# Kernel optimization log

Measured on AMD Instinct MI355X. Metric: run time of the kernel, lower is better.

## Reference

```python
import jax, jax.numpy as jnp
import numpy as np

D_IN = 2048
D_SAE = 16384
BATCH = 4096


def setup_inputs() -> dict:
    key = jax.random.key(0)
    kx, kw, kb, kt, kd = jax.random.split(key, 5)
    x = jax.random.normal(kx, (BATCH, D_IN), dtype=jnp.float32)
    # kaiming-uniform-like init for encoder weight [d_sae, d_in]
    bound = float(np.sqrt(6.0 / D_IN))
    W_enc = jax.random.uniform(kw, (D_SAE, D_IN), minval=-bound, maxval=bound, dtype=jnp.float32)
    b_enc = jnp.zeros((D_SAE,), dtype=jnp.float32)
    # decoder weight [d_in, d_sae]; use small random values instead of the
    # zeros init so the reference output is non-degenerate
    W_dec = jax.random.normal(kd, (D_IN, D_SAE), dtype=jnp.float32) * 0.02
    # learnable per-feature thresholds tau (tau_init=0.0 plus jitter)
    tau = jax.random.normal(kt, (D_SAE,), dtype=jnp.float32) * 0.01
    return {"x": x, "W_enc": W_enc, "b_enc": b_enc, "tau": tau, "W_dec": W_dec, "k_cap": 64}


def reference(x, W_enc, b_enc, tau, W_dec, k_cap):
    # encode: pre = x @ W_enc.T + b_enc  -> [B, d_sae]
    pre = jnp.einsum('bi,si->bs', x, W_enc) + b_enc
    # JumpReLU gate: y = relu(pre - tau), mask = (pre > tau)
    codes = jax.nn.relu(pre - tau)
    mask = (pre > tau).astype(pre.dtype)
    # top-k cap (gate_mode='jumprelu_cap'): keep codes >= k-th largest per row
    k = min(k_cap, codes.shape[1])
    vals = jax.lax.top_k(codes, k)[0]          # [B, k], sorted desc
    kth = vals[:, -1:]                          # [B, 1]
    mask_k = (codes >= kth).astype(codes.dtype)
    codes = codes * mask_k
    mask = mask * mask_k
    # decode: recon = codes @ W_dec.T  -> [B, d_in]
    recon = jnp.einsum('bs,is->bi', codes, W_dec)
    return recon, codes, mask
```

## Files before the change

### kernel.cpp

```cpp
#include <hip/hip_runtime.h>

#define D_IN   2048
#define D_SAE  16384
#define BATCH  4096
#define CAP    256
#define MAXB   64
#define DELTA  1e-2f

typedef __attribute__((ext_vector_type(8))) _Float16 f16x8;
typedef __attribute__((ext_vector_type(4))) _Float16 f16x4;
typedef __attribute__((ext_vector_type(4))) float f32x4;

__global__ __launch_bounds__(256) void to_f16_2(const float* __restrict__ in1,
                                                ushort* __restrict__ out1, int n14,
                                                const float* __restrict__ in2,
                                                ushort* __restrict__ out2, int n24) {
    int i = blockIdx.x * blockDim.x + threadIdx.x;
    int stride = gridDim.x * blockDim.x;
    int total = n14 + n24;
    for (; i < total; i += stride) {
        const float4* src = (i < n14) ? ((const float4*)in1 + i)
                                      : ((const float4*)in2 + (i - n14));
        ushort4* dst = (i < n14) ? ((ushort4*)out1 + i)
                                 : ((ushort4*)out2 + (i - n14));
        float4 v = *src;
        ushort4 h;
        float*  vp = (float*)&v;
        ushort* hp = (ushort*)&h;
        #pragma unroll
        for (int j = 0; j < 4; ++j) {
            _Float16 f = (_Float16)vp[j];
            hp[j] = *(ushort*)&f;
        }
        *dst = h;
    }
}

__device__ __forceinline__ void async_copy16(const void* g, void* l) {
    __builtin_amdgcn_global_load_lds(
        (const __attribute__((address_space(1))) unsigned int*)g,
        (__attribute__((address_space(3))) unsigned int*)l, 16, 0, 0);
}

template<int F16OUT>
__global__ __launch_bounds__(512) void gemm_enc_mfma(
        const ushort* __restrict__ xh,
        const ushort* __restrict__ wh,
        const float* __restrict__ b_enc,
        const float* __restrict__ tau,
        void* __restrict__ rawout) {
    __shared__ ushort lds9[9][8192];

    const int tid  = threadIdx.x;
    const int w    = tid >> 6;
    const int lane = tid & 63;
    const int wm   = w >> 2;
    const int wn   = w & 3;
    const int m0 = blockIdx.x * 256;
    const int s0 = blockIdx.y * 256;

    const int fr = lane & 15;
    const int fq = lane >> 4;

    const int srow0 = w * 8 + (lane >> 3);
    const int srow1 = 64 + srow0;
    const int sc0i  = (((lane & 7) - srow0) & 7) * 8;

    const ushort* panelA = xh + (size_t)m0 * 2048;
    const ushort* panelB = wh + (size_t)s0 * 2048;

    auto stage_unit = [&](int slot, int ab, int h, int koff) {
        const ushort* gp = (ab == 0) ? panelA : panelB;
        const ushort* g0 = gp + (size_t)(h * 128 + srow0) * 2048 + koff + sc0i;
        const ushort* g1 = gp + (size_t)(h * 128 + srow1) * 2048 + koff + sc0i;
        async_copy16(g0, &lds9[slot][w * 512]);
        async_copy16(g1, &lds9[slot][4096 + w * 512]);
    };

    int a_off[8][2], b_off[4][2];
    #pragma unroll
    for (int m = 0; m < 8; ++m) {
        int r = m * 16 + fr;
        #pragma unroll
        for (int kk = 0; kk < 2; ++kk)
            a_off[m][kk] = r * 64 + (((kk * 4 + fq) + r) & 7) * 8;
    }
    #pragma unroll
    for (int g = 0; g < 4; ++g) {
        int r = (wn & 1) * 64 + g * 16 + fr;
        #pragma unroll
        for (int kk = 0; kk < 2; ++kk)
            b_off[g][kk] = r * 64 + (((kk * 4 + fq) + r) & 7) * 8;
    }

    f32x4 acc[8][4] = {};

    stage_unit(0, 0, 0, 0);
    stage_unit(1, 1, 0, 0);
    stage_unit(2, 1, 1, 0);
    stage_unit(3, 0, 1, 0);
    stage_unit(4, 0, 0, 64);

    const int wmu = wm ? 3 : 0;
    const int wbu = 1 + (wn >> 1);

#define STG(P)                                                                 \
    do {                                                                       \
        int u_ = 4 * t + (P) + 5;                                              \
        if (u_ < 128) {                                                        \
            int ui_ = u_ & 3;                                                  \
            stage_unit(u_ % 9, (ui_ == 0 || ui_ == 3) ? 0 : 1,                 \
                       (ui_ >= 2) ? 1 : 0, (u_ >> 2) * 64);                    \
        }                                                                      \
    } while (0)

#define PHASE(QM, QN, P)                                                       \
    do {                                                                       \
        STG(P);                                                                \
        if ((P) == 0) {                                                        \
            if (t != 31) asm volatile("s_waitcnt vmcnt(4)" ::: "memory");      \
            else         asm volatile("s_waitcnt vmcnt(0)" ::: "memory");      \
        }                                                                      \
        asm volatile("s_barrier" ::: "memory");                                \
        f16x8 af[4][2], bf[2][2];                                              \
        _Pragma("unroll") for (int mm = 0; mm < 4; ++mm)                       \
            _Pragma("unroll") for (int kk = 0; kk < 2; ++kk)                   \
                af[mm][kk] = *(const f16x8*)&ldsA[a_off[(QM) * 4 + mm][kk]];   \
        _Pragma("unroll") for (int nn = 0; nn < 2; ++nn)                       \
            _Pragma("unroll") for (int kk = 0; kk < 2; ++kk)                   \
                bf[nn][kk] = *(const f16x8*)&ldsB[b_off[(QN) * 2 + nn][kk]];   \
        __builtin_amdgcn_s_setprio(1);                                         \
        _Pragma("unroll") for (int kk = 0; kk < 2; ++kk)                       \
            _Pragma("unroll") for (int mm = 0; mm < 4; ++mm)                   \
                _Pragma("unroll") for (int nn = 0; nn < 2; ++nn)               \
                    acc[(QM) * 4 + mm][(QN) * 2 + nn] =                        \
                        __builtin_amdgcn_mfma_f32_16x16x32_f16(                \
                            af[mm][kk], bf[nn][kk],                            \
                            acc[(QM) * 4 + mm][(QN) * 2 + nn], 0, 0, 0);       \
        __builtin_amdgcn_s_setprio(0);                                         \
        asm volatile("s_barrier" ::: "memory");                                \
    } while (0)

    for (int t = 0; t < 32; ++t) {
        const ushort* ldsA = &lds9[(4 * t + wmu) % 9][0];
        const ushort* ldsB = &lds9[(4 * t + wbu) % 9][0];
        PHASE(0, 0, 0);
        PHASE(0, 1, 1);
        PHASE(1, 0, 2);
        PHASE(1, 1, 3);
    }
#undef PHASE
#undef STG

    float bias[4];
    int col[4];
    #pragma unroll
    for (int n = 0; n < 4; ++n) {
        col[n] = s0 + wn * 64 + n * 16 + fr;
        bias[n] = b_enc[col[n]] - tau[col[n]];
    }
    #pragma unroll
    for (int m = 0; m < 8; ++m) {
        int rbase = m0 + wm * 128 + m * 16 + fq * 4;
        #pragma unroll
        for (int n = 0; n < 4; ++n) {
            #pragma unroll
            for (int r = 0; r < 4; ++r) {
                float v = fmaxf(acc[m][n][r] + bias[n], 0.f);
                size_t ofs = (size_t)(rbase + r) * D_SAE + col[n];
                if (F16OUT) {
                    _Float16 hv = (_Float16)v;
                    ((ushort*)rawout)[ofs] = *(ushort*)&hv;
                } else {
                    ((float*)rawout)[ofs] = v;
                }
            }
        }
    }
}

__global__ __launch_bounds__(256) void transpose_wdec_f16(const float* __restrict__ W_dec,
                                                          _Float16* __restrict__ W_decT) {
    __shared__ float t[64][65];
    const int tid = threadIdx.x;
    const int x0 = blockIdx.x * 64;
    const int y0 = blockIdx.y * 64;
    const int tx = tid & 15;
    const int ty = tid >> 4;
    #pragma unroll
    for (int p = 0; p < 4; ++p) {
        float4 v = *(const float4*)&W_dec[(size_t)(y0 + p * 16 + ty) * D_SAE + x0 + tx * 4];
        t[p * 16 + ty][tx * 4 + 0] = v.x;
        t[p * 16 + ty][tx * 4 + 1] = v.y;
        t[p * 16 + ty][tx * 4 + 2] = v.z;
        t[p * 16 + ty][tx * 4 + 3] = v.w;
    }
    __syncthreads();
    #pragma unroll
    for (int p = 0; p < 4; ++p) {
        int s = p * 16 + ty;
        f16x4 o;
        #pragma unroll
        for (int q = 0; q < 4; ++q)
            o[q] = (_Float16)t[tx * 4 + q][s];
        *(f16x4*)&W_decT[(size_t)(x0 + s) * D_IN + y0 + tx * 4] = o;
    }
}

__device__ __forceinline__ int block_incl_scan(int v, int tid, int* wtot, int* pT) {
    const int lane = tid & 63, wid = tid >> 6;
    int s = v;
    #pragma unroll
    for (int off = 1; off < 64; off <<= 1) {
        int n = __shfl_up(s, off, 64);
        if (lane >= off) s += n;
    }
    if (lane == 63) wtot[wid] = s;
    __syncthreads();
    int pre = 0, T = 0;
    #pragma unroll
    for (int w2 = 0; w2 < 4; ++w2) {
        int t = wtot[w2];
        T += t;
        if (w2 < wid) pre += t;
    }
    __syncthreads();
    *pT = T;
    return s + pre;
}

template<int SRC16>
__global__ __launch_bounds__(256) void select_apply(
        const void* __restrict__ rawsrc,
        float* __restrict__ codes, float* __restrict__ mask,
        const int* __restrict__ kptr,
        const float* __restrict__ x, const float* __restrict__ W_enc,
        const float* __restrict__ b_enc, const float* __restrict__ tau,
        int* __restrict__ cnt_out, int* __restrict__ idx_out,
        float* __restrict__ val_out) {
    const int row = blockIdx.x;
    const int tid = threadIdx.x;
    const int wid = tid >> 6;
    const long base = (long)row * D_SAE;

    float c[8][8];
    if (SRC16) {
        const ushort* rh = (const ushort*)rawsrc;
        #pragma unroll
        for (int i = 0; i < 8; ++i) {
            uint4 u = *(const uint4*)(rh + base + i * 2048 + tid * 8);
            const unsigned* up = (const unsigned*)&u;
            #pragma unroll
            for (int q = 0; q < 4; ++q) {
                ushort b0 = (ushort)(up[q] & 0xFFFFu), b1 = (ushort)(up[q] >> 16);
                _Float16 h0, h1;
                *(ushort*)&h0 = b0; *(ushort*)&h1 = b1;
                c[i][2 * q]     = (float)h0;
                c[i][2 * q + 1] = (float)h1;
            }
        }
    } else {
        const float* rf = (const float*)rawsrc;
        #pragma unroll
        for (int i = 0; i < 8; ++i) {
            float4 v0 = *(const float4*)(rf + base + i * 2048 + tid * 8);
            float4 v1 = *(const float4*)(rf + base + i * 2048 + tid * 8 + 4);
            c[i][0] = v0.x; c[i][1] = v0.y; c[i][2] = v0.z; c[i][3] = v0.w;
            c[i][4] = v1.x; c[i][5] = v1.y; c[i][6] = v1.z; c[i][7] = v1.w;
        }
    }

    int K = kptr[0];
    if (K > D_SAE) K = D_SAE;

    __shared__ int    hist4[4][1024];
    __shared__ int    hist1c[64];
    __shared__ int    wtot[4];
    __shared__ int    bidx[MAXB];
    __shared__ double exactv[MAXB];
    __shared__ int    selfl[MAXB];
    __shared__ double dsum[4];
    __shared__ int    sh_B, sh_nAB, sh_kpat;

    #pragma unroll
    for (int q = 0; q < 16; ++q) ((int*)hist4)[tid + q * 256] = 0;
    if (tid < 64) hist1c[tid] = 0;
    if (tid == 0) { sh_B = -1; sh_nAB = 0; }
    __syncthreads();
    #pragma unroll
    for (int i = 0; i < 8; ++i)
        #pragma unroll
        for (int j = 0; j < 8; ++j) {
            _Float16 h = (_Float16)c[i][j];
            ushort pat = *(ushort*)&h;
            if (pat) atomicAdd(&hist4[wid][pat >> 6], 1);
        }
    __syncthreads();

    int mh[4];
    int s_loc = 0;
    #pragma unroll
    for (int q = 0; q < 4; ++q) {
        mh[q] = hist4[0][4 * tid + q] + hist4[1][4 * tid + q]
              + hist4[2][4 * tid + q] + hist4[3][4 * tid + q];
        s_loc += mh[q];
    }
    int T1;
    int incl1 = block_incl_scan(s_loc, tid, wtot, &T1);
    int I = T1 - (incl1 - s_loc);
    int E = I - s_loc;
    if (I >= K && E < K) {
        int cnt = E, b;
        for (b = 3; b > 0; --b) {
            cnt += mh[b];
            if (cnt >= K) break;
        }
        if (cnt < K) { cnt += mh[0]; b = 0; }
        sh_B = 4 * tid + b;
        sh_nAB = cnt - mh[b];
    }
    __syncthreads();
    const int B = sh_B, nAB = sh_nAB;

    if (B >= 0) {
        #pragma unroll
        for (int i = 0; i < 8; ++i)
            #pragma unroll
            for (int j = 0; j < 8; ++j) {
                _Float16 h = (_Float16)c[i][j];
                ushort pat = *(ushort*)&h;
                if (pat && (int)(pat >> 6) == B) atomicAdd(&hist1c[pat & 63], 1);
            }
    }
    __syncthreads();
    if (tid == 0) {
        int kpat = 0;
        if (B >= 0) {
            int cnt = nAB, l;
            for (l = 63; l >= 0; --l) {
                cnt += hist1c[l];
                if (cnt >= K) break;
            }
            if (l < 0) l = 0;
            kpat = (B << 6) | l;
        }
        sh_kpat = kpat;
    }
    __syncthreads();
    _Float16 kh; *(ushort*)&kh = (ushort)sh_kpat;
    const float kf = (float)kh;
    const float thr_hi = kf + DELTA;
    const float thr_lo = kf - DELTA;

    int cA = 0, cB2 = 0;
    #pragma unroll
    for (int i = 0; i < 8; ++i)
        #pragma unroll
        for (int j = 0; j < 8; ++j) {
            float cc = c[i][j];
            cA  += (cc > thr_hi);
            cB2 += (cc >= thr_lo) && (cc <= thr_hi);
        }
    int pv = (cB2 << 16) | cA;
    int T2;
    int incl2 = block_incl_scan(pv, tid, wtot, &T2);
    int excl2 = incl2 - pv;
    const int nA = T2 & 0xFFFF;
    int posB = excl2 >> 16;
    int nb   = T2 >> 16;
    if (nb > MAXB) nb = MAXB;

    {
        int p = posB;
        #pragma unroll
        for (int i = 0; i < 8; ++i)
            #pragma unroll
            for (int j = 0; j < 8; ++j) {
                float cc = c[i][j];
                if ((cc >= thr_lo) && (cc <= thr_hi)) {
                    if (p < MAXB) bidx[p] = i * 2048 + tid * 8 + j;
                    ++p;
                }
            }
    }
    __syncthreads();

    const float* xrow = x + (size_t)row * D_IN;
    for (int jj = 0; jj < nb; ++jj) {
        int s = bidx[jj];
        const float* wrow = W_enc + (size_t)s * D_IN;
        double a = 0.0;
        #pragma unroll
        for (int q = 0; q < 8; ++q)
            a += (double)xrow[tid * 8 + q] * (double)wrow[tid * 8 + q];
        #pragma unroll
        for (int off = 32; off; off >>= 1) a += __shfl_xor(a, off, 64);
        if ((tid & 63) == 0) dsum[tid >> 6] = a;
        __syncthreads();
        if (tid == 0)
            exactv[jj] = dsum[0] + dsum[1] + dsum[2] + dsum[3]
                         + (double)b_enc[s] - (double)tau[s];
        __syncthreads();
    }

    int m = K - nA;
    if (m > nb) m = nb;
    if (tid < nb) {
        double e = exactv[tid];
        int rank = 0;
        for (int l = 0; l < nb; ++l) rank += (exactv[l] > e);
        selfl[tid] = (rank < m) ? 1 : 0;
    }
    __syncthreads();

    unsigned long long ov = 0ull;
    for (int jj = 0; jj < nb; ++jj) {
        int s = bidx[jj];
        if (((s >> 3) & 255) == tid && selfl[jj])
            ov |= 1ull << (((s >> 11) << 3) | (s & 7));
    }

    int kc = 0;
    #pragma unroll
    for (int i = 0; i < 8; ++i)
        #pragma unroll
        for (int j = 0; j < 8; ++j) {
            float cc = c[i][j];
            bool sel = (cc > thr_hi) || ((ov >> (i * 8 + j)) & 1ull);
            kc += sel && (cc > 0.f);
        }
    int T3;
    int incl3 = block_incl_scan(kc, tid, wtot, &T3);
    int pos   = incl3 - kc;
    int total = T3;

    #pragma unroll
    for (int i = 0; i < 8; ++i) {
        f32x4 cf0, cf1, mf0, mf1;
        #pragma unroll
        for (int j = 0; j < 8; ++j) {
            float cc = c[i][j];
            bool sel = (cc > thr_hi) || ((ov >> (i * 8 + j)) & 1ull);
            bool m_  = sel && (cc > 0.f);
            float cv = sel ? cc : 0.f;
            float mv = m_ ? 1.f : 0.f;
            if (j < 4) { cf0[j] = cv; mf0[j] = mv; }
            else       { cf1[j - 4] = cv; mf1[j - 4] = mv; }
            if (m_) {
                if (pos < CAP) {
                    idx_out[row * CAP + pos] = i * 2048 + tid * 8 + j;
                    val_out[row * CAP + pos] = cv;
                }
                ++pos;
            }
        }
        long o = base + i * 2048 + tid * 8;
        __builtin_nontemporal_store(cf0, (f32x4*)(codes + o));
        __builtin_nontemporal_store(cf1, (f32x4*)(codes + o + 4));
        __builtin_nontemporal_store(mf0, (f32x4*)(mask + o));
        __builtin_nontemporal_store(mf1, (f32x4*)(mask + o + 4));
    }
    if (tid == 0) cnt_out[row] = total < CAP ? total : CAP;
}

__global__ __launch_bounds__(256) void recon_sparse(const _Float16* __restrict__ Wd16,
                                                    const int* __restrict__ cnt,
                                                    const int* __restrict__ idx,
                                                    const float* __restrict__ val,
                                                    float* __restrict__ recon) {
    const int row  = blockIdx.x >> 1;
    const int half = blockIdx.x & 1;
    const int tid  = threadIdx.x;
    __shared__ int   s_idx[CAP];
    __shared__ float s_val[CAP];
    const int n = cnt[row];
    for (int j = tid; j < n; j += 256) {
        s_idx[j] = idx[row * CAP + j];
        s_val[j] = val[row * CAP + j];
    }
    __syncthreads();

    const int colb = half * 1024 + tid * 4;
    float4 a = {0.f, 0.f, 0.f, 0.f};
    for (int j = 0; j < n; ++j) {
        float c = s_val[j];
        f16x4 w0 = *(const f16x4*)(Wd16 + (size_t)s_idx[j] * D_IN + colb);
        a.x = fmaf(c, (float)w0[0], a.x); a.y = fmaf(c, (float)w0[1], a.y);
        a.z = fmaf(c, (float)w0[2], a.z); a.w = fmaf(c, (float)w0[3], a.w);
    }
    *(float4*)(recon + (size_t)row * D_IN + colb) = a;
}

extern "C" void kernel_launch(void* const* d_in, const int* in_sizes, int n_in,
                              void* d_out, int out_size, void* d_ws, size_t ws_size,
                              hipStream_t stream) {
    const float* x     = (const float*)d_in[0];
    const float* W_enc = (const float*)d_in[1];
    const float* b_enc = (const float*)d_in[2];
    const float* tau   = (const float*)d_in[3];
    const float* W_dec = (const float*)d_in[4];
    const int*   kptr  = (const int*)d_in[5];

    float* recon = (float*)d_out;
    float* codes = recon + (size_t)BATCH * D_IN;
    float* maskp = codes + (size_t)BATCH * D_SAE;

    char* w = (char*)d_ws;
    const size_t OFF_X   = (size_t)D_SAE * D_IN * 2;
    const size_t OFF_RAW = OFF_X + (size_t)BATCH * D_IN * 2;
    const size_t RAWSZ   = (size_t)BATCH * D_SAE * 2;
    const size_t TAILSZ  = 16384 + 2 * (size_t)BATCH * CAP * 4;
    const bool f16raw = ws_size >= OFF_RAW + RAWSZ + TAILSZ;

    const size_t OFF_CNT = f16raw ? (OFF_RAW + RAWSZ) : OFF_RAW;
    ushort*   w_f16  = (ushort*)w;
    ushort*   x_f16  = (ushort*)(w + OFF_X);
    _Float16* W_decT = (_Float16*)w;
    int*      cnt    = (int*)  (w + OFF_CNT);
    int*      idxl   = (int*)  (w + OFF_CNT + 16384);
    float*    vall   = (float*)(w + OFF_CNT + 16384 + (size_t)BATCH * CAP * 4);
    void*     raw    = f16raw ? (void*)(w + OFF_RAW) : (void*)codes;

    hipLaunchKernelGGL(to_f16_2, dim3(2560), dim3(256), 0, stream,
                       x, x_f16, BATCH * D_IN / 4,
                       W_enc, w_f16, D_SAE * D_IN / 4);
    if (f16raw) {
        hipLaunchKernelGGL((gemm_enc_mfma<1>), dim3(BATCH / 256, D_SAE / 256), dim3(512), 0, stream,
                           x_f16, w_f16, b_enc, tau, raw);
        hipLaunchKernelGGL((select_apply<1>), dim3(BATCH), dim3(256), 0, stream,
                           raw, codes, maskp, kptr, x, W_enc, b_enc, tau, cnt, idxl, vall);
    } else {
        hipLaunchKernelGGL((gemm_enc_mfma<0>), dim3(BATCH / 256, D_SAE / 256), dim3(512), 0, stream,
                           x_f16, w_f16, b_enc, tau, raw);
        hipLaunchKernelGGL((select_apply<0>), dim3(BATCH), dim3(256), 0, stream,
                           raw, codes, maskp, kptr, x, W_enc, b_enc, tau, cnt, idxl, vall);
    }
    hipLaunchKernelGGL(transpose_wdec_f16, dim3(D_SAE / 64, D_IN / 64), dim3(256), 0, stream,
                       W_dec, W_decT);
    hipLaunchKernelGGL(recon_sparse, dim3(BATCH * 2), dim3(256), 0, stream,
                       W_decT, cnt, idxl, vall, recon);
}
```

Measured before the change: 692.1 us.

## Fuse sparse decoder reconstruction into the select kernel via shared-memory index lists

```diff
diff --git a/kernel.cpp b/kernel.cpp
--- a/kernel.cpp
+++ b/kernel.cpp
@@ -230,14 +230,14 @@
 }
 
 template<int SRC16>
-__global__ __launch_bounds__(256) void select_apply(
+__global__ __launch_bounds__(256) void select_recon(
         const void* __restrict__ rawsrc,
         float* __restrict__ codes, float* __restrict__ mask,
         const int* __restrict__ kptr,
         const float* __restrict__ x, const float* __restrict__ W_enc,
         const float* __restrict__ b_enc, const float* __restrict__ tau,
-        int* __restrict__ cnt_out, int* __restrict__ idx_out,
-        float* __restrict__ val_out) {
+        const _Float16* __restrict__ Wd16,
+        float* __restrict__ recon) {
     const int row = blockIdx.x;
     const int tid = threadIdx.x;
     const int wid = tid >> 6;
@@ -281,6 +281,8 @@
     __shared__ int    selfl[MAXB];
     __shared__ double dsum[4];
     __shared__ int    sh_B, sh_nAB, sh_kpat;
+    __shared__ int    s_idx[CAP];
+    __shared__ float  s_val[CAP];
 
     #pragma unroll
     for (int q = 0; q < 16; ++q) ((int*)hist4)[tid + q * 256] = 0;
@@ -431,8 +433,7 @@
         }
     int T3;
     int incl3 = block_incl_scan(kc, tid, wtot, &T3);
-    int pos   = incl3 - kc;
-    int total = T3;
+    int pos = incl3 - kc;
 
     #pragma unroll
     for (int i = 0; i < 8; ++i) {
@@ -448,8 +449,8 @@
             else       { cf1[j - 4] = cv; mf1[j - 4] = mv; }
             if (m_) {
                 if (pos < CAP) {
-                    idx_out[row * CAP + pos] = i * 2048 + tid * 8 + j;
-                    val_out[row * CAP + pos] = cv;
+                    s_idx[pos] = i * 2048 + tid * 8 + j;
+                    s_val[pos] = cv;
                 }
                 ++pos;
             }
@@ -460,35 +461,24 @@
         __builtin_nontemporal_store(mf0, (f32x4*)(mask + o));
         __builtin_nontemporal_store(mf1, (f32x4*)(mask + o + 4));
     }
-    if (tid == 0) cnt_out[row] = total < CAP ? total : CAP;
-}
-
-__global__ __launch_bounds__(256) void recon_sparse(const _Float16* __restrict__ Wd16,
-                                                    const int* __restrict__ cnt,
-                                                    const int* __restrict__ idx,
-                                                    const float* __restrict__ val,
-                                                    float* __restrict__ recon) {
-    const int row  = blockIdx.x >> 1;
-    const int half = blockIdx.x & 1;
-    const int tid  = threadIdx.x;
-    __shared__ int   s_idx[CAP];
-    __shared__ float s_val[CAP];
-    const int n = cnt[row];
-    for (int j = tid; j < n; j += 256) {
-        s_idx[j] = idx[row * CAP + j];
-        s_val[j] = val[row * CAP + j];
-    }
-    __syncthreads();
-
-    const int colb = half * 1024 + tid * 4;
-    float4 a = {0.f, 0.f, 0.f, 0.f};
+    __syncthreads();
+
+    const int n = (T3 < CAP) ? T3 : CAP;
+    float4 a0 = {0.f, 0.f, 0.f, 0.f};
+    float4 a1 = {0.f, 0.f, 0.f, 0.f};
     for (int j = 0; j < n; ++j) {
-        float c = s_val[j];
-        f16x4 w0 = *(const f16x4*)(Wd16 + (size_t)s_idx[j] * D_IN + colb);
-        a.x = fmaf(c, (float)w0[0], a.x); a.y = fmaf(c, (float)w0[1], a.y);
-        a.z = fmaf(c, (float)w0[2], a.z); a.w = fmaf(c, (float)w0[3], a.w);
-    }
-    *(float4*)(recon + (size_t)row * D_IN + colb) = a;
+        float cv = s_val[j];
+        const _Float16* wp = Wd16 + (size_t)s_idx[j] * D_IN;
+        f16x4 w0 = *(const f16x4*)(wp + tid * 4);
+        f16x4 w1 = *(const f16x4*)(wp + 1024 + tid * 4);
+        a0.x = fmaf(cv, (float)w0[0], a0.x); a0.y = fmaf(cv, (float)w0[1], a0.y);
+        a0.z = fmaf(cv, (float)w0[2], a0.z); a0.w = fmaf(cv, (float)w0[3], a0.w);
+        a1.x = fmaf(cv, (float)w1[0], a1.x); a1.y = fmaf(cv, (float)w1[1], a1.y);
+        a1.z = fmaf(cv, (float)w1[2], a1.z); a1.w = fmaf(cv, (float)w1[3], a1.w);
+    }
+    float* out = recon + (size_t)row * D_IN;
+    *(float4*)(out + tid * 4)        = a0;
+    *(float4*)(out + 1024 + tid * 4) = a1;
 }
 
 extern "C" void kernel_launch(void* const* d_in, const int* in_sizes, int n_in,
@@ -509,16 +499,11 @@
     const size_t OFF_X   = (size_t)D_SAE * D_IN * 2;
     const size_t OFF_RAW = OFF_X + (size_t)BATCH * D_IN * 2;
     const size_t RAWSZ   = (size_t)BATCH * D_SAE * 2;
-    const size_t TAILSZ  = 16384 + 2 * (size_t)BATCH * CAP * 4;
-    const bool f16raw = ws_size >= OFF_RAW + RAWSZ + TAILSZ;
-
-    const size_t OFF_CNT = f16raw ? (OFF_RAW + RAWSZ) : OFF_RAW;
+    const bool f16raw = ws_size >= OFF_RAW + RAWSZ;
+
     ushort*   w_f16  = (ushort*)w;
     ushort*   x_f16  = (ushort*)(w + OFF_X);
     _Float16* W_decT = (_Float16*)w;
-    int*      cnt    = (int*)  (w + OFF_CNT);
-    int*      idxl   = (int*)  (w + OFF_CNT + 16384);
-    float*    vall   = (float*)(w + OFF_CNT + 16384 + (size_t)BATCH * CAP * 4);
     void*     raw    = f16raw ? (void*)(w + OFF_RAW) : (void*)codes;
 
     hipLaunchKernelGGL(to_f16_2, dim3(2560), dim3(256), 0, stream,
@@ -527,16 +512,16 @@
     if (f16raw) {
         hipLaunchKernelGGL((gemm_enc_mfma<1>), dim3(BATCH / 256, D_SAE / 256), dim3(512), 0, stream,
                            x_f16, w_f16, b_enc, tau, raw);
-        hipLaunchKernelGGL((select_apply<1>), dim3(BATCH), dim3(256), 0, stream,
-                           raw, codes, maskp, kptr, x, W_enc, b_enc, tau, cnt, idxl, vall);
+        hipLaunchKernelGGL(transpose_wdec_f16, dim3(D_SAE / 64, D_IN / 64), dim3(256), 0, stream,
+                           W_dec, W_decT);
+        hipLaunchKernelGGL((select_recon<1>), dim3(BATCH), dim3(256), 0, stream,
+                           raw, codes, maskp, kptr, x, W_enc, b_enc, tau, W_decT, recon);
     } else {
         hipLaunchKernelGGL((gemm_enc_mfma<0>), dim3(BATCH / 256, D_SAE / 256), dim3(512), 0, stream,
                            x_f16, w_f16, b_enc, tau, raw);
-        hipLaunchKernelGGL((select_apply<0>), dim3(BATCH), dim3(256), 0, stream,
-                           raw, codes, maskp, kptr, x, W_enc, b_enc, tau, cnt, idxl, vall);
-    }
-    hipLaunchKernelGGL(transpose_wdec_f16, dim3(D_SAE / 64, D_IN / 64), dim3(256), 0, stream,
-                       W_dec, W_decT);
-    hipLaunchKernelGGL(recon_sparse, dim3(BATCH * 2), dim3(256), 0, stream,
-                       W_decT, cnt, idxl, vall, recon);
-}
+        hipLaunchKernelGGL(transpose_wdec_f16, dim3(D_SAE / 64, D_IN / 64), dim3(256), 0, stream,
+                           W_dec, W_decT);
+        hipLaunchKernelGGL((select_recon<0>), dim3(BATCH), dim3(256), 0, stream,
+                           raw, codes, maskp, kptr, x, W_enc, b_enc, tau, W_decT, recon);
+    }
+}
```

Result: faster. 654.1 us (median of 2 runs) (-5.5%).
